# Kernel tuning notes

Hardware: AMD Instinct MI355X
Metric: run time of the kernel (lower is better)

Reference implementation:

```python
import jax, jax.numpy as jnp
import numpy as np
import math

D_MODEL = 512
N_HEADS = 8
HEAD_DIM = D_MODEL // N_HEADS


def setup_inputs() -> dict:
    key = jax.random.key(0)
    k1, k2, k3 = jax.random.split(key, 3)
    B, T = 2, 4096
    x = jax.random.normal(k1, (B, T, D_MODEL), dtype=jnp.float32)
    # nn.Linear weights: stored as [out, in], applied as x @ W.T
    W_QKV = jax.random.normal(k2, (3 * D_MODEL, D_MODEL), dtype=jnp.float32) * (1.0 / math.sqrt(D_MODEL))
    W_O = jax.random.normal(k3, (D_MODEL, D_MODEL), dtype=jnp.float32) * (1.0 / math.sqrt(D_MODEL))
    return {"x": x, "W_QKV": W_QKV, "W_O": W_O}


def reference(x, W_QKV, W_O):
    B, T, C = x.shape
    qkv = (x @ W_QKV.T).reshape(B, T, 3, N_HEADS, HEAD_DIM)
    q, k, v = qkv[:, :, 0], qkv[:, :, 1], qkv[:, :, 2]  # [B,T,H,D]
    # scores: [B,H,T,T]
    scale = math.sqrt(HEAD_DIM)
    attn = jnp.einsum('bqhd,bkhd->bhqk', q, k) / scale
    causal_mask = jnp.triu(jnp.ones((T, T), dtype=bool), k=1)
    attn = jnp.where(causal_mask, -jnp.inf, attn)
    attn = jax.nn.softmax(attn, axis=-1)
    out = jnp.einsum('bhqk,bkhd->bqhd', attn, v).reshape(B, T, C)
    return out @ W_O.T
```

## Files before the change

kernel.cpp:

```cpp
#include <hip/hip_runtime.h>
#include <hip/hip_bf16.h>

typedef __bf16 bf16_t;
typedef __bf16 bf16x8 __attribute__((ext_vector_type(8)));
typedef __bf16 bf16x4 __attribute__((ext_vector_type(4)));
typedef float  floatx4 __attribute__((ext_vector_type(4)));

static __device__ __forceinline__ floatx4 mfma16(bf16x8 a, bf16x8 b, floatx4 c) {
  return __builtin_amdgcn_mfma_f32_16x16x32_bf16(a, b, c, 0, 0, 0);
}

typedef __attribute__((address_space(3))) void lds_vp;
typedef __attribute__((address_space(1))) void glb_vp;
#define GLDS16(g, l) \
  __builtin_amdgcn_global_load_lds((glb_vp*)(g), (lds_vp*)(l), 16, 0, 0)

__global__ void cvt_all_kernel(const float* __restrict__ x,
                               const float* __restrict__ wqkv,
                               const float* __restrict__ wo,
                               bf16_t* __restrict__ xb,
                               bf16_t* __restrict__ wqkvb,
                               bf16_t* __restrict__ wob) {
  int i = blockIdx.x * blockDim.x + threadIdx.x;
  const float4* src; bf16x4* dst; int off;
  if (i < 1048576)      { src = (const float4*)x;    dst = (bf16x4*)xb;    off = i; }
  else if (i < 1245184) { src = (const float4*)wqkv; dst = (bf16x4*)wqkvb; off = i - 1048576; }
  else                  { src = (const float4*)wo;   dst = (bf16x4*)wob;   off = i - 1245184; }
  float4 v = src[off];
  bf16x4 o;
  o[0] = (bf16_t)v.x; o[1] = (bf16_t)v.y; o[2] = (bf16_t)v.z; o[3] = (bf16_t)v.w;
  dst[off] = o;
}

__global__ __launch_bounds__(256) void gemm_qkv(
    const bf16_t* __restrict__ A, const bf16_t* __restrict__ B,
    bf16_t* __restrict__ Qo, bf16_t* __restrict__ Ko, bf16_t* __restrict__ Vto)
{
  __shared__ __align__(16) bf16_t As[2][128 * 64];
  __shared__ __align__(16) bf16_t Bs[2][128 * 64];
  const int tid  = threadIdx.x;
  const int lane = tid & 63;
  const int w    = tid >> 6;
  const int quad = lane >> 4;
  const int l15  = lane & 15;
  const int l7   = lane & 7;
  const int wm   = w & 1;
  const int wn   = w >> 1;
  const int K    = 512;

  floatx4 acc[4][4];
  #pragma unroll
  for (int i = 0; i < 4; ++i)
    #pragma unroll
    for (int j = 0; j < 4; ++j)
      acc[i][j] = (floatx4){0.f, 0.f, 0.f, 0.f};

  const bf16_t* Ab = A + (size_t)blockIdx.x * 128 * K;
  const bf16_t* Bb = B + (size_t)blockIdx.y * 128 * K;

  auto stage = [&](int buf, int k0) {
    #pragma unroll
    for (int i = 0; i < 4; ++i) {
      int c = tid + 256 * i;
      int row = c >> 3, colc = c & 7;
      int gofs = ((colc ^ (row & 7)) << 3);
      GLDS16(&Ab[(size_t)row * K + k0 + gofs], &As[buf][c * 8]);
      GLDS16(&Bb[(size_t)row * K + k0 + gofs], &Bs[buf][c * 8]);
    }
  };

  stage(0, 0);
  for (int it = 0; it < 8; ++it) {
    const int cur = it & 1;
    __syncthreads();
    if (it + 1 < 8) stage(cur ^ 1, (it + 1) << 6);
    #pragma unroll
    for (int ks = 0; ks < 2; ++ks) {
      bf16x8 af[4], bfr[4];
      #pragma unroll
      for (int t = 0; t < 4; ++t) {
        af[t]  = *(const bf16x8*)&As[cur][(wm * 64 + t * 16 + l15) * 64 +
                                         (((ks * 4 + quad) ^ l7) << 3)];
        bfr[t] = *(const bf16x8*)&Bs[cur][(wn * 64 + t * 16 + l15) * 64 +
                                         (((ks * 4 + quad) ^ l7) << 3)];
      }
      #pragma unroll
      for (int mt = 0; mt < 4; ++mt)
        #pragma unroll
        for (int nt = 0; nt < 4; ++nt)
          acc[mt][nt] = mfma16(af[mt], bfr[nt], acc[mt][nt]);
    }
  }

  if (blockIdx.y < 8) {
    #pragma unroll
    for (int mt = 0; mt < 4; ++mt) {
      #pragma unroll
      for (int nt = 0; nt < 4; ++nt) {
        #pragma unroll
        for (int r = 0; r < 4; ++r) {
          int m = blockIdx.x * 128 + wm * 64 + mt * 16 + quad * 4 + r;
          int n = blockIdx.y * 128 + wn * 64 + nt * 16 + l15;
          float v = acc[mt][nt][r];
          int b = m >> 12, t = m & 4095;
          int h = (n >> 6) & 7, d = n & 63;
          size_t bh = (size_t)(b * 8 + h);
          if (n < 512)
            Qo[bh * 262144 + (size_t)t * 64 + d] = (bf16_t)(v * 0.18033688f);
          else
            Ko[bh * 262144 + (size_t)t * 64 + d] = (bf16_t)v;
        }
      }
    }
  } else {
    __syncthreads();
    bf16_t* L = &As[0][0];
    #pragma unroll
    for (int mt = 0; mt < 4; ++mt)
      #pragma unroll
      for (int nt = 0; nt < 4; ++nt) {
        int n_l = wn * 64 + nt * 16 + l15;
        int mc  = wm * 8 + mt * 2 + (quad >> 1);
        bf16x4 v4;
        #pragma unroll
        for (int r = 0; r < 4; ++r) v4[r] = (bf16_t)acc[mt][nt][r];
        *(bf16x4*)&L[n_l * 128 + ((mc ^ (n_l & 15)) << 3) + (quad & 1) * 4] = v4;
      }
    __syncthreads();
    const int t0 = (blockIdx.x & 31) * 128;
    const int b  = blockIdx.x >> 5;
    #pragma unroll
    for (int i = 0; i < 8; ++i) {
      int c = tid + 256 * i;
      int n_l = c >> 4, tc = c & 15;
      int h = ((blockIdx.y - 8) << 1) | (n_l >> 6);
      int d = n_l & 63;
      size_t bh = (size_t)(b * 8 + h);
      int base0 = (tc >> 2) * 32 + (tc & 3) * 4;
      bf16x4 lo = *(const bf16x4*)&L[n_l * 128 +
                     (((base0 >> 3) ^ (n_l & 15)) << 3) + (base0 & 7)];
      bf16x4 hi = *(const bf16x4*)&L[n_l * 128 +
                     ((((base0 + 16) >> 3) ^ (n_l & 15)) << 3) + (base0 & 7)];
      bf16x8 o;
      #pragma unroll
      for (int e = 0; e < 4; ++e) { o[e] = lo[e]; o[e + 4] = hi[e]; }
      *(bf16x8*)&Vto[bh * 262144 + (size_t)d * 4096 + t0 + tc * 8] = o;
    }
  }
}

__global__ __launch_bounds__(256) void gemm_out(
    const bf16_t* __restrict__ A, const bf16_t* __restrict__ B,
    float* __restrict__ Cf)
{
  __shared__ __align__(16) bf16_t As[2][64 * 64];
  __shared__ __align__(16) bf16_t Bs[2][128 * 64];
  const int tid  = threadIdx.x;
  const int lane = tid & 63;
  const int w    = tid >> 6;
  const int quad = lane >> 4;
  const int l15  = lane & 15;
  const int l7   = lane & 7;

  floatx4 acc[4][2];
  #pragma unroll
  for (int i = 0; i < 4; ++i)
    #pragma unroll
    for (int j = 0; j < 2; ++j)
      acc[i][j] = (floatx4){0.f, 0.f, 0.f, 0.f};

  const bf16_t* Ab = A + (size_t)blockIdx.x * 64 * 512;
  const bf16_t* Bb = B + (size_t)blockIdx.y * 128 * 512;

  auto stage = [&](int buf, int k0) {
    #pragma unroll
    for (int i = 0; i < 2; ++i) {
      int c = tid + 256 * i;
      int row = c >> 3, colc = c & 7;
      GLDS16(&Ab[(size_t)row * 512 + k0 + ((colc ^ (row & 7)) << 3)],
             &As[buf][c * 8]);
    }
    #pragma unroll
    for (int i = 0; i < 4; ++i) {
      int c = tid + 256 * i;
      int row = c >> 3, colc = c & 7;
      GLDS16(&Bb[(size_t)row * 512 + k0 + ((colc ^ (row & 7)) << 3)],
             &Bs[buf][c * 8]);
    }
  };

  stage(0, 0);
  for (int it = 0; it < 8; ++it) {
    const int cur = it & 1;
    __syncthreads();
    if (it + 1 < 8) stage(cur ^ 1, (it + 1) << 6);
    #pragma unroll
    for (int ks = 0; ks < 2; ++ks) {
      bf16x8 af[4], bfr[2];
      #pragma unroll
      for (int t = 0; t < 4; ++t)
        af[t]  = *(const bf16x8*)&As[cur][(t * 16 + l15) * 64 +
                                         (((ks * 4 + quad) ^ l7) << 3)];
      #pragma unroll
      for (int t = 0; t < 2; ++t)
        bfr[t] = *(const bf16x8*)&Bs[cur][(w * 32 + t * 16 + l15) * 64 +
                                         (((ks * 4 + quad) ^ l7) << 3)];
      #pragma unroll
      for (int mt = 0; mt < 4; ++mt)
        #pragma unroll
        for (int nt = 0; nt < 2; ++nt)
          acc[mt][nt] = mfma16(af[mt], bfr[nt], acc[mt][nt]);
    }
  }

  #pragma unroll
  for (int mt = 0; mt < 4; ++mt)
    #pragma unroll
    for (int nt = 0; nt < 2; ++nt)
      #pragma unroll
      for (int r = 0; r < 4; ++r) {
        int m = blockIdx.x * 64 + mt * 16 + quad * 4 + r;
        int n = blockIdx.y * 128 + w * 32 + nt * 16 + l15;
        Cf[(size_t)m * 512 + n] = acc[mt][nt][r];
      }
}

__global__ __launch_bounds__(256, 4) void attn_kernel(
    const bf16_t* __restrict__ Qg, const bf16_t* __restrict__ Kgl,
    const bf16_t* __restrict__ Vtg, bf16_t* __restrict__ Og)
{
  __shared__ __align__(16) bf16_t Ks[2][64 * 64];
  __shared__ __align__(16) bf16_t Vts[2][64 * 64];

  const int tid  = threadIdx.x;
  const int lane = tid & 63;
  const int w    = tid >> 6;
  const int quad = lane >> 4;
  const int l15  = lane & 15;

  const int id = blockIdx.x;
  const int k8 = id & 7;
  const int j  = id >> 3;
  const int bh = 2 * k8 + (j & 1);
  const int jj = j >> 1;
  const int u  = jj & 15, rr = jj >> 4;
  const int qt = (rr == 0) ? u : (rr == 1) ? 63 - u : (rr == 2) ? 31 - u : 32 + u;
  const size_t bh_off = (size_t)bh * 262144;
  const int b = bh >> 3, h = bh & 7;

  const int gq = qt * 64 + w * 16 + l15;
  bf16x8 aq0, aq1;
  {
    const bf16_t* Qp = Qg + bh_off + (size_t)gq * 64;
    aq0 = *(const bf16x8*)&Qp[quad * 8];
    aq1 = *(const bf16x8*)&Qp[32 + quad * 8];
  }
  bf16x8 ones;
  #pragma unroll
  for (int i = 0; i < 8; ++i) ones[i] = (bf16_t)1.0f;

  floatx4 acc_o[4], acc_l;
  #pragma unroll
  for (int dt = 0; dt < 4; ++dt) acc_o[dt] = (floatx4){0.f, 0.f, 0.f, 0.f};
  acc_l = (floatx4){0.f, 0.f, 0.f, 0.f};

  auto stage = [&](int buf, int kt) {
    const bf16_t* Kp = Kgl + bh_off + (size_t)kt * 4096;
    const bf16_t* Vp = Vtg + bh_off + (size_t)kt * 64;
    #pragma unroll
    for (int i = 0; i < 2; ++i) {
      int c = tid + 256 * i;
      int row = c >> 3, colc = c & 7;
      GLDS16(&Kp[row * 64 + ((colc ^ (row & 7)) << 3)], &Ks[buf][c * 8]);
    }
    #pragma unroll
    for (int i = 0; i < 2; ++i) {
      int c = tid + 256 * i;
      int row = c >> 3, colc = c & 7;
      GLDS16(&Vp[(size_t)row * 4096 + ((colc ^ (row & 7)) << 3)], &Vts[buf][c * 8]);
    }
  };

  stage(0, 0);
  const int nkt = qt + 1;
  for (int kt = 0; kt < nkt; ++kt) {
    const int cur = kt & 1;
    __syncthreads();
    if (kt + 1 < nkt) stage(cur ^ 1, kt + 1);

    floatx4 s[4];
    #pragma unroll
    for (int nt = 0; nt < 4; ++nt) s[nt] = (floatx4){0.f, 0.f, 0.f, 0.f};
    #pragma unroll
    for (int nt = 0; nt < 4; ++nt) {
      bf16x8 bk0 = *(const bf16x8*)&Ks[cur][(nt * 16 + l15) * 64 +
                                           ((quad ^ (l15 & 7)) << 3)];
      s[nt] = mfma16(bk0, aq0, s[nt]);
    }
    #pragma unroll
    for (int nt = 0; nt < 4; ++nt) {
      bf16x8 bk1 = *(const bf16x8*)&Ks[cur][(nt * 16 + l15) * 64 +
                                           (((4 + quad) ^ (l15 & 7)) << 3)];
      s[nt] = mfma16(bk1, aq1, s[nt]);
    }

    if (kt == qt) {
      #pragma unroll
      for (int nt = 0; nt < 4; ++nt)
        #pragma unroll
        for (int r = 0; r < 4; ++r)
          if (kt * 64 + nt * 16 + quad * 4 + r > gq) s[nt][r] = -3.0e38f;
    }
    #pragma unroll
    for (int nt = 0; nt < 4; ++nt)
      #pragma unroll
      for (int r = 0; r < 4; ++r)
        s[nt][r] = exp2f(s[nt][r]);

    #pragma unroll
    for (int kc = 0; kc < 2; ++kc) {
      bf16x8 pb;
      #pragma unroll
      for (int r = 0; r < 4; ++r) {
        pb[r]     = (bf16_t)s[kc * 2][r];
        pb[r + 4] = (bf16_t)s[kc * 2 + 1][r];
      }
      acc_l = mfma16(ones, pb, acc_l);
      #pragma unroll
      for (int dt = 0; dt < 4; ++dt) {
        int row = dt * 16 + l15;
        bf16x8 av = *(const bf16x8*)&Vts[cur][row * 64 +
                                             (((kc * 4 + quad) ^ (l15 & 7)) << 3)];
        acc_o[dt] = mfma16(av, pb, acc_o[dt]);
      }
    }
  }

  __syncthreads();
  bf16_t* Ot = &Ks[0][0];
  const float rl = 1.0f / acc_l[0];
  const int t_own = w * 16 + l15;
  #pragma unroll
  for (int dt = 0; dt < 4; ++dt) {
    bf16x4 o4;
    #pragma unroll
    for (int r = 0; r < 4; ++r) o4[r] = (bf16_t)(acc_o[dt][r] * rl);
    *(bf16x4*)&Ot[t_own * 64 +
                  (((dt * 2 + (quad >> 1)) ^ (t_own & 7)) << 3) + (quad & 1) * 4] = o4;
  }
  __syncthreads();
  #pragma unroll
  for (int i = 0; i < 2; ++i) {
    int cc = tid + 256 * i;
    int t = cc >> 3, c = cc & 7;
    bf16x8 o8 = *(const bf16x8*)&Ot[t * 64 + ((c ^ (t & 7)) << 3)];
    int trow = qt * 64 + t;
    *(bf16x8*)&Og[((size_t)b * 4096 + trow) * 512 + h * 64 + c * 8] = o8;
  }
}

extern "C" void kernel_launch(void* const* d_in, const int* in_sizes, int n_in,
                              void* d_out, int out_size, void* d_ws, size_t ws_size,
                              hipStream_t stream) {
  const float* x    = (const float*)d_in[0];
  const float* wqkv = (const float*)d_in[1];
  const float* wo   = (const float*)d_in[2];
  float* out = (float*)d_out;

  char* ws = (char*)d_ws;
  bf16_t* xb    = (bf16_t*)(ws);
  bf16_t* wqkvb = (bf16_t*)(ws + 8388608);
  bf16_t* wob   = (bf16_t*)(ws + 9961472);
  bf16_t* Qb    = (bf16_t*)(ws + 10485760);
  bf16_t* Kb    = (bf16_t*)(ws + 18874368);
  bf16_t* Vtb   = (bf16_t*)(ws + 27262976);
  bf16_t* Ob    = xb;

  cvt_all_kernel<<<5120, 256, 0, stream>>>(x, wqkv, wo, xb, wqkvb, wob);

  gemm_qkv<<<dim3(64, 12), 256, 0, stream>>>(xb, wqkvb, Qb, Kb, Vtb);
  attn_kernel<<<1024, 256, 0, stream>>>(Qb, Kb, Vtb, Ob);
  gemm_out<<<dim3(128, 4), 256, 0, stream>>>(Ob, wob, out);
}
```

Before: 172.4 us.

## Make attention persistent with atomic work queue and split-K across wave halves

```diff
diff --git a/kernel.cpp b/kernel.cpp
--- a/kernel.cpp
+++ b/kernel.cpp
@@ -225,137 +225,165 @@
       }
 }
 
-__global__ __launch_bounds__(256, 4) void attn_kernel(
+__global__ __launch_bounds__(512, 4) void attn_kernel(
     const bf16_t* __restrict__ Qg, const bf16_t* __restrict__ Kgl,
-    const bf16_t* __restrict__ Vtg, bf16_t* __restrict__ Og)
+    const bf16_t* __restrict__ Vtg, bf16_t* __restrict__ Og,
+    unsigned int* __restrict__ counter)
 {
-  __shared__ __align__(16) bf16_t Ks[2][64 * 64];
-  __shared__ __align__(16) bf16_t Vts[2][64 * 64];
-
-  const int tid  = threadIdx.x;
-  const int lane = tid & 63;
-  const int w    = tid >> 6;
-  const int quad = lane >> 4;
-  const int l15  = lane & 15;
-
-  const int id = blockIdx.x;
-  const int k8 = id & 7;
-  const int j  = id >> 3;
-  const int bh = 2 * k8 + (j & 1);
-  const int jj = j >> 1;
-  const int u  = jj & 15, rr = jj >> 4;
-  const int qt = (rr == 0) ? u : (rr == 1) ? 63 - u : (rr == 2) ? 31 - u : 32 + u;
-  const size_t bh_off = (size_t)bh * 262144;
-  const int b = bh >> 3, h = bh & 7;
-
-  const int gq = qt * 64 + w * 16 + l15;
-  bf16x8 aq0, aq1;
-  {
-    const bf16_t* Qp = Qg + bh_off + (size_t)gq * 64;
-    aq0 = *(const bf16x8*)&Qp[quad * 8];
-    aq1 = *(const bf16x8*)&Qp[32 + quad * 8];
-  }
+  __shared__ __align__(16) bf16_t Ks[2][128 * 64];
+  __shared__ __align__(16) bf16_t Vts[2][64 * 128];
+  __shared__ int nxslot;
+
+  const int tid   = threadIdx.x;
+  const int lane  = tid & 63;
+  const int w     = tid >> 6;
+  const int khalf = w >> 2;
+  const int ws    = w & 3;
+  const int quad  = lane >> 4;
+  const int l15   = lane & 15;
+
   bf16x8 ones;
   #pragma unroll
   for (int i = 0; i < 8; ++i) ones[i] = (bf16_t)1.0f;
 
-  floatx4 acc_o[4], acc_l;
-  #pragma unroll
-  for (int dt = 0; dt < 4; ++dt) acc_o[dt] = (floatx4){0.f, 0.f, 0.f, 0.f};
-  acc_l = (floatx4){0.f, 0.f, 0.f, 0.f};
-
-  auto stage = [&](int buf, int kt) {
-    const bf16_t* Kp = Kgl + bh_off + (size_t)kt * 4096;
-    const bf16_t* Vp = Vtg + bh_off + (size_t)kt * 64;
+  auto stage = [&](int buf, size_t bhoff, int kt) {
+    const bf16_t* Kp = Kgl + bhoff + (size_t)kt * 8192;
+    const bf16_t* Vp = Vtg + bhoff + (size_t)kt * 128;
     #pragma unroll
     for (int i = 0; i < 2; ++i) {
-      int c = tid + 256 * i;
+      int c = tid + 512 * i;
       int row = c >> 3, colc = c & 7;
       GLDS16(&Kp[row * 64 + ((colc ^ (row & 7)) << 3)], &Ks[buf][c * 8]);
     }
     #pragma unroll
     for (int i = 0; i < 2; ++i) {
-      int c = tid + 256 * i;
-      int row = c >> 3, colc = c & 7;
-      GLDS16(&Vp[(size_t)row * 4096 + ((colc ^ (row & 7)) << 3)], &Vts[buf][c * 8]);
+      int c = tid + 512 * i;
+      int row = c >> 4, colc = c & 15;
+      GLDS16(&Vp[(size_t)row * 4096 + ((colc ^ (row & 15)) << 3)], &Vts[buf][c * 8]);
     }
   };
 
-  stage(0, 0);
-  const int nkt = qt + 1;
-  for (int kt = 0; kt < nkt; ++kt) {
-    const int cur = kt & 1;
-    __syncthreads();
-    if (kt + 1 < nkt) stage(cur ^ 1, kt + 1);
-
-    floatx4 s[4];
-    #pragma unroll
-    for (int nt = 0; nt < 4; ++nt) s[nt] = (floatx4){0.f, 0.f, 0.f, 0.f};
-    #pragma unroll
-    for (int nt = 0; nt < 4; ++nt) {
-      bf16x8 bk0 = *(const bf16x8*)&Ks[cur][(nt * 16 + l15) * 64 +
-                                           ((quad ^ (l15 & 7)) << 3)];
-      s[nt] = mfma16(bk0, aq0, s[nt]);
-    }
-    #pragma unroll
-    for (int nt = 0; nt < 4; ++nt) {
-      bf16x8 bk1 = *(const bf16x8*)&Ks[cur][(nt * 16 + l15) * 64 +
-                                           (((4 + quad) ^ (l15 & 7)) << 3)];
-      s[nt] = mfma16(bk1, aq1, s[nt]);
-    }
-
-    if (kt == qt) {
+  int item = blockIdx.x;
+  int buf  = 0;
+  stage(0, (size_t)(item & 15) * 262144, 0);
+
+  while (item < 1024) {
+    const int qt  = 63 - (item >> 4);
+    const int bh  = item & 15;
+    const size_t bh_off = (size_t)bh * 262144;
+    const int b = bh >> 3, h = bh & 7;
+    const int nkt = (qt >> 1) + 1;
+    const int gq  = qt * 64 + ws * 16 + l15;
+
+    bf16x8 aq0, aq1;
+    {
+      const bf16_t* Qp = Qg + bh_off + (size_t)gq * 64;
+      aq0 = *(const bf16x8*)&Qp[quad * 8];
+      aq1 = *(const bf16x8*)&Qp[32 + quad * 8];
+    }
+    if (tid == 0) nxslot = 512 + (int)atomicAdd(counter, 1u);
+
+    floatx4 acc_o[4], acc_l;
+    #pragma unroll
+    for (int dt = 0; dt < 4; ++dt) acc_o[dt] = (floatx4){0.f, 0.f, 0.f, 0.f};
+    acc_l = (floatx4){0.f, 0.f, 0.f, 0.f};
+
+    int nxt = 1024;
+    for (int kt = 0; kt < nkt; ++kt) {
+      __syncthreads();
+      const int nb = buf ^ 1;
+      if (kt + 1 < nkt) {
+        stage(nb, bh_off, kt + 1);
+      } else {
+        nxt = nxslot;
+        if (nxt < 1024)
+          stage(nb, (size_t)(nxt & 15) * 262144, 0);
+      }
+
+      floatx4 s[4];
+      #pragma unroll
+      for (int nt = 0; nt < 4; ++nt) s[nt] = (floatx4){0.f, 0.f, 0.f, 0.f};
+      #pragma unroll
+      for (int nt = 0; nt < 4; ++nt) {
+        bf16x8 bk0 = *(const bf16x8*)&Ks[buf][(khalf * 64 + nt * 16 + l15) * 64 +
+                                             ((quad ^ (l15 & 7)) << 3)];
+        s[nt] = mfma16(bk0, aq0, s[nt]);
+      }
+      #pragma unroll
+      for (int nt = 0; nt < 4; ++nt) {
+        bf16x8 bk1 = *(const bf16x8*)&Ks[buf][(khalf * 64 + nt * 16 + l15) * 64 +
+                                             (((4 + quad) ^ (l15 & 7)) << 3)];
+        s[nt] = mfma16(bk1, aq1, s[nt]);
+      }
+
+      if (kt == nkt - 1) {
+        #pragma unroll
+        for (int nt = 0; nt < 4; ++nt)
+          #pragma unroll
+          for (int r = 0; r < 4; ++r)
+            if (kt * 128 + khalf * 64 + nt * 16 + quad * 4 + r > gq)
+              s[nt][r] = -3.0e38f;
+      }
       #pragma unroll
       for (int nt = 0; nt < 4; ++nt)
         #pragma unroll
         for (int r = 0; r < 4; ++r)
-          if (kt * 64 + nt * 16 + quad * 4 + r > gq) s[nt][r] = -3.0e38f;
-    }
-    #pragma unroll
-    for (int nt = 0; nt < 4; ++nt)
-      #pragma unroll
-      for (int r = 0; r < 4; ++r)
-        s[nt][r] = exp2f(s[nt][r]);
-
-    #pragma unroll
-    for (int kc = 0; kc < 2; ++kc) {
-      bf16x8 pb;
-      #pragma unroll
-      for (int r = 0; r < 4; ++r) {
-        pb[r]     = (bf16_t)s[kc * 2][r];
-        pb[r + 4] = (bf16_t)s[kc * 2 + 1][r];
-      }
-      acc_l = mfma16(ones, pb, acc_l);
+          s[nt][r] = exp2f(s[nt][r]);
+
+      #pragma unroll
+      for (int kc = 0; kc < 2; ++kc) {
+        bf16x8 pb;
+        #pragma unroll
+        for (int r = 0; r < 4; ++r) {
+          pb[r]     = (bf16_t)s[kc * 2][r];
+          pb[r + 4] = (bf16_t)s[kc * 2 + 1][r];
+        }
+        acc_l = mfma16(ones, pb, acc_l);
+        const int kcg = khalf * 2 + kc;
+        #pragma unroll
+        for (int dt = 0; dt < 4; ++dt) {
+          bf16x8 av = *(const bf16x8*)&Vts[buf][(dt * 16 + l15) * 128 +
+                                               (((kcg * 4 + quad) ^ l15) << 3)];
+          acc_o[dt] = mfma16(av, pb, acc_o[dt]);
+        }
+      }
+      buf = nb;
+    }
+
+    const int sb = buf ^ 1;
+    float*  scr = (float*)&Ks[sb][0];
+    float*  scl = (float*)((char*)&Vts[sb][0] + 8192);
+    bf16_t* Ot  = &Vts[sb][0];
+    __syncthreads();
+    if (khalf == 1) {
+      #pragma unroll
+      for (int dt = 0; dt < 4; ++dt)
+        *(floatx4*)&scr[(((ws * 4 + dt) * 64) + lane) * 4] = acc_o[dt];
+      scl[ws * 64 + lane] = acc_l[0];
+    }
+    __syncthreads();
+    if (khalf == 0) {
+      #pragma unroll
+      for (int dt = 0; dt < 4; ++dt)
+        acc_o[dt] += *(const floatx4*)&scr[(((ws * 4 + dt) * 64) + lane) * 4];
+      float rl = 1.0f / (acc_l[0] + scl[ws * 64 + lane]);
+      const int t_own = ws * 16 + l15;
       #pragma unroll
       for (int dt = 0; dt < 4; ++dt) {
-        int row = dt * 16 + l15;
-        bf16x8 av = *(const bf16x8*)&Vts[cur][row * 64 +
-                                             (((kc * 4 + quad) ^ (l15 & 7)) << 3)];
-        acc_o[dt] = mfma16(av, pb, acc_o[dt]);
-      }
-    }
-  }
-
-  __syncthreads();
-  bf16_t* Ot = &Ks[0][0];
-  const float rl = 1.0f / acc_l[0];
-  const int t_own = w * 16 + l15;
-  #pragma unroll
-  for (int dt = 0; dt < 4; ++dt) {
-    bf16x4 o4;
-    #pragma unroll
-    for (int r = 0; r < 4; ++r) o4[r] = (bf16_t)(acc_o[dt][r] * rl);
-    *(bf16x4*)&Ot[t_own * 64 +
-                  (((dt * 2 + (quad >> 1)) ^ (t_own & 7)) << 3) + (quad & 1) * 4] = o4;
-  }
-  __syncthreads();
-  #pragma unroll
-  for (int i = 0; i < 2; ++i) {
-    int cc = tid + 256 * i;
-    int t = cc >> 3, c = cc & 7;
-    bf16x8 o8 = *(const bf16x8*)&Ot[t * 64 + ((c ^ (t & 7)) << 3)];
-    int trow = qt * 64 + t;
-    *(bf16x8*)&Og[((size_t)b * 4096 + trow) * 512 + h * 64 + c * 8] = o8;
+        bf16x4 o4;
+        #pragma unroll
+        for (int r = 0; r < 4; ++r) o4[r] = (bf16_t)(acc_o[dt][r] * rl);
+        *(bf16x4*)&Ot[t_own * 64 +
+                      (((dt * 2 + (quad >> 1)) ^ (t_own & 7)) << 3) + (quad & 1) * 4] = o4;
+      }
+    }
+    __syncthreads();
+    {
+      int t = tid >> 3, c = tid & 7;
+      bf16x8 o8 = *(const bf16x8*)&Ot[t * 64 + ((c ^ (t & 7)) << 3)];
+      *(bf16x8*)&Og[((size_t)b * 4096 + qt * 64 + t) * 512 + h * 64 + c * 8] = o8;
+    }
+    item = nxt;
   }
 }
 
@@ -374,11 +402,13 @@
   bf16_t* Qb    = (bf16_t*)(ws + 10485760);
   bf16_t* Kb    = (bf16_t*)(ws + 18874368);
   bf16_t* Vtb   = (bf16_t*)(ws + 27262976);
+  unsigned int* counter = (unsigned int*)(ws + 35651584);
   bf16_t* Ob    = xb;
 
   cvt_all_kernel<<<5120, 256, 0, stream>>>(x, wqkv, wo, xb, wqkvb, wob);
 
   gemm_qkv<<<dim3(64, 12), 256, 0, stream>>>(xb, wqkvb, Qb, Kb, Vtb);
-  attn_kernel<<<1024, 256, 0, stream>>>(Qb, Kb, Vtb, Ob);
+  hipMemsetAsync(counter, 0, 4, stream);
+  attn_kernel<<<512, 512, 0, stream>>>(Qb, Kb, Vtb, Ob, counter);
   gemm_out<<<dim3(128, 4), 256, 0, stream>>>(Ob, wob, out);
 }
```

New measurement: 188.3 us. +9.2%, slower.
